# Performance work log

Hardware: AMD Instinct MI355X
Metric: run time of the kernel (lower is better)

## Reference

```python
import jax, jax.numpy as jnp
import numpy as np

K_SIZE = 5
EPS = 1e-6
EPS_L = 1e-3
EPS_W = 1e-3


def setup_inputs() -> dict:
    key = jax.random.key(0)
    k1, k2, k3 = jax.random.split(key, 3)
    B, H, W = 4, 512, 512
    return {
        "input": jax.random.normal(k1, (B, 1, H, W), jnp.float32),
        "L_params": jax.random.normal(k2, (B, H, W, 3), jnp.float32),
        "w": jax.random.normal(k3, (B, 2, H, W), jnp.float32),
    }


def _bilinear(img, py, px):
    # img: (B,H,W); py,px: (B,K,H,W) absolute sample coords. Zero outside bounds
    # (matches torchvision deform_conv2d zero-padded bilinear sampling).
    B, H, W = img.shape
    y0 = jnp.floor(py)
    x0 = jnp.floor(px)
    wy = py - y0  # fractional weights
    wx = px - x0
    bidx = jnp.arange(B)[:, None, None, None]

    def corner(yc, xc, wgt):
        valid = (yc >= 0) & (yc <= H - 1) & (xc >= 0) & (xc <= W - 1)
        yi = jnp.clip(yc, 0, H - 1).astype(jnp.int32)
        xi = jnp.clip(xc, 0, W - 1).astype(jnp.int32)
        return jnp.where(valid, img[bidx, yi, xi] * wgt, 0.0)

    return (corner(y0, x0, (1 - wy) * (1 - wx))
            + corner(y0, x0 + 1, (1 - wy) * wx)
            + corner(y0 + 1, x0, wy * (1 - wx))
            + corner(y0 + 1, x0 + 1, wy * wx))


def reference(input, L_params, w):
    B, C, H, W = input.shape
    n = K_SIZE  # n_theta = ceil(sqrt(k*k)) = k

    # --- per-pixel 2x2 metric M = L L^T, L = [[a,0],[b,c]] ---
    a = jnp.abs(L_params[..., 0]) + EPS_L
    b = L_params[..., 1]
    c = jnp.abs(L_params[..., 2]) + EPS_L
    M00 = a * a            # (B,H,W)
    M01 = a * b            # = M10
    M11 = b * b + c * c

    # --- inverse of (M + eps*I), closed-form 2x2 ---
    d00 = M00 + EPS
    d11 = M11 + EPS
    det = d00 * d11 - M01 * M01
    I00 = d11 / det
    I01 = -M01 / det
    I11 = d00 / det

    # --- w rescaled so its M^{-1}-norm is < 1 (Randers condition) ---
    wx_ = w[:, 0]
    wy_ = w[:, 1]
    q = I00 * wx_ * wx_ + 2 * I01 * wx_ * wy_ + I11 * wy_ * wy_
    norm = jnp.sqrt(q + EPS)                                  # (B,H,W)
    tuned = (jax.nn.sigmoid(norm) - 0.5) * 2.0 * (1.0 - EPS_W)
    wt = w * (tuned / (norm + EPS))[:, None]                  # (B,2,H,W)

    # --- Randers unit-ball tangent sampling pattern ---
    theta = jnp.arange(0.0, 2.0 * np.pi - EPS, 2.0 * np.pi / n)  # (n,)
    ct = jnp.cos(theta)[None, :, None, None]  # (1,n,1,1)
    st = jnp.sin(theta)[None, :, None, None]
    # F(u) = sqrt(u^T M u) + <w,u>
    quad = (M00[:, None] * ct * ct + 2.0 * M01[:, None] * ct * st
            + M11[:, None] * st * st)                         # (B,n,H,W)
    F = jnp.sqrt(quad) + wt[:, 0:1] * ct + wt[:, 1:2] * st    # (B,n,H,W)
    yx = ct / (F + EPS)  # boundary point of unit Randers ball, x comp
    yy = st / (F + EPS)  # y comp

    s_interp = (jnp.arange(n, dtype=jnp.float32) + 1.0) / n   # (n,)
    s5 = s_interp[None, :, None, None, None]
    dy = (s5 * yy[:, None]).reshape(B, n * n, H, W)           # (B,K,H,W)
    dx = (s5 * yx[:, None]).reshape(B, n * n, H, W)

    gy = jnp.arange(H, dtype=jnp.float32)[None, None, :, None] + dy
    gx = jnp.arange(W, dtype=jnp.float32)[None, None, None, :] + dx

    samp = _bilinear(input[:, 0], gy, gx)                     # (B,K,H,W)
    # uniform deform-conv kernel weight 1/n^2; sample_centre=False => no centre term
    out = samp.sum(axis=1)[:, None] / float(n * n)            # (B,1,H,W)
    return out
```

## Files before the change

### kernel.cpp

```cpp
#include <hip/hip_runtime.h>
#include <math.h>

#define K_SIZE 5
#define EPS    1e-6f
#define EPS_L  1e-3f
#define EPS_W  1e-3f

#define BATCH 4
#define HGT   512
#define WID   512
#define HW    (HGT * WID)

#define ENT        513
#define ROW_ENTRIES 520
#define ROW_BYTES  (ROW_ENTRIES * 8)
#define IMG_BYTES  (ENT * ROW_BYTES)
#define TBL_BYTES  ((size_t)BATCH * IMG_BYTES)

typedef int int32x4 __attribute__((ext_vector_type(4)));
typedef float floatx2 __attribute__((ext_vector_type(2)));
typedef _Float16 half4v __attribute__((ext_vector_type(4)));
typedef _Float16 half2v __attribute__((ext_vector_type(2)));

__device__ float llvm_amdgcn_raw_buffer_load_fp32(int32x4 srsrc, int voffset,
                                                  int soffset, int aux)
    __asm("llvm.amdgcn.raw.buffer.load.f32");
__device__ floatx2 llvm_amdgcn_raw_buffer_load_2fp32(int32x4 srsrc, int voffset,
                                                     int soffset, int aux)
    __asm("llvm.amdgcn.raw.buffer.load.v2f32");

__global__ __launch_bounds__(256) void pack_kernel(
    const float* __restrict__ input, char* __restrict__ tbl)
{
    const int t = blockIdx.x * blockDim.x + threadIdx.x;
    if (t >= BATCH * ENT * ENT) return;
    const int k  = t % ENT;
    const int ri = (t / ENT) % ENT;
    const int b  = t / (ENT * ENT);

    const float* __restrict__ img = input + (size_t)b * HW;

    const bool top = (ri >= 1), bot = (ri <= HGT - 1);
    const bool lef = (k  >= 1), rig = (k  <= WID - 1);
    const int yT = (ri - 1) << 9;
    const int yB = ri << 9;

    union { half4v h; floatx2 f; } cv;
    cv.h.x = (_Float16)((top && lef) ? img[yT + k - 1] : 0.0f);
    cv.h.y = (_Float16)((top && rig) ? img[yT + k]     : 0.0f);
    cv.h.z = (_Float16)((bot && lef) ? img[yB + k - 1] : 0.0f);
    cv.h.w = (_Float16)((bot && rig) ? img[yB + k]     : 0.0f);

    floatx2* dst = (floatx2*)(tbl + (size_t)b * IMG_BYTES + (size_t)ri * ROW_BYTES + ((size_t)k << 3));
    *dst = cv.f;
}

__global__ __launch_bounds__(256) void fused_sample_kernel_f16(
    const char* __restrict__ tbl,
    const float* __restrict__ Lp,
    const float* __restrict__ wbuf,
    float* __restrict__ out)
{
#pragma clang fp contract(off)
    const int idx = blockIdx.x * blockDim.x + threadIdx.x;

    const int b = blockIdx.x >> 10;
    const int p = idx & (HW - 1);
    const int y = p >> 9;
    const int x = p & (WID - 1);

    union {
        struct { const void* base; unsigned num; unsigned cfg; } s;
        int32x4 v;
    } desc;
    desc.s.base = (const void*)(tbl + (size_t)b * IMG_BYTES);
    desc.s.num  = (unsigned)IMG_BYTES;
    desc.s.cfg  = 0x00020000u;
    const int32x4 rsrc = desc.v;

    const size_t l_off = (size_t)idx * 3;
    const float L0 = Lp[l_off + 0];
    const float L1 = Lp[l_off + 1];
    const float L2 = Lp[l_off + 2];

    const float a  = fabsf(L0) + EPS_L;
    const float bb = L1;
    const float c  = fabsf(L2) + EPS_L;

    const float M00 = a * a;
    const float M01 = a * bb;
    const float M11 = (bb * bb) + (c * c);

    const float d00 = M00 + EPS;
    const float d11 = M11 + EPS;
    const float det = (d00 * d11) - (M01 * M01);
    const float I00 = d11 / det;
    const float I01 = (-M01) / det;
    const float I11 = d00 / det;

    const float wx = wbuf[(size_t)b * 2 * HW + p];
    const float wy = wbuf[(size_t)b * 2 * HW + HW + p];

    const float q    = (((I00 * wx) * wx) + (((2.0f * I01) * wx) * wy)) + ((I11 * wy) * wy);
    const float norm = sqrtf(q + EPS);

    const float e    = (float)exp((double)(-norm));
    const float sig  = 1.0f / (1.0f + e);
    const float tuned = ((sig - 0.5f) * 2.0f) * (1.0f - EPS_W);
    const float scale = tuned / (norm + EPS);
    const float wtx = wx * scale;
    const float wty = wy * scale;

    const float CT[K_SIZE] = { 1.0f,  0.30901696090f, -0.80901703575f, -0.80901693229f,  0.30901712828f };
    const float ST[K_SIZE] = { 0.0f,  0.95105652717f,  0.58778519534f, -0.58778533774f, -0.95105647279f };
    const float SV[K_SIZE] = { 0.2f, 0.4f, 0.6f, 0.8f, 1.0f };

    const float fy = (float)y;
    const float fx = (float)x;

    float acc0 = 0.0f;
    float acc1 = 0.0f;

    #pragma unroll
    for (int k = 0; k < K_SIZE; ++k) {
        const float ct = CT[k];
        const float st = ST[k];
        const float quad = (((M00 * ct) * ct) + (((2.0f * M01) * ct) * st)) + ((M11 * st) * st);
        const float F    = (sqrtf(quad) + (wtx * ct)) + (wty * st);
        const float Fe   = F + EPS;
        const float rFe  = __builtin_amdgcn_rcpf(Fe);
        const float yx   = ct * rFe;
        const float yy   = st * rFe;

        #pragma unroll
        for (int s = 0; s < K_SIZE; ++s) {
            const float sv = SV[s];
            const float gy = fmaf(sv, yy, fy);
            const float gx = fmaf(sv, yx, fx);

            const int   y0i = (int)floorf(gy);
            const int   x0i = (int)floorf(gx);
            const float wyf = __builtin_amdgcn_fractf(gy);
            const float wxf = __builtin_amdgcn_fractf(gx);

            const int ri = y0i + 1;
            const int ke = min(max(x0i + 1, 0), ENT - 1);
            const unsigned off = (unsigned)ri * (unsigned)ROW_BYTES + ((unsigned)ke << 3);

            const floatx2 pf = llvm_amdgcn_raw_buffer_load_2fp32(rsrc, (int)off, 0, 0);
            union { floatx2 f; half4v h; } cv;
            cv.f = pf;
            const float v00 = (float)cv.h.x;
            const float v01 = (float)cv.h.y;
            const float v10 = (float)cv.h.z;
            const float v11 = (float)cv.h.w;

            const bool vx0 = (unsigned)x0i < (unsigned)WID;
            const bool vx1 = (unsigned)(x0i + 1) < (unsigned)WID;
            const float zx0 = vx0 ? (1.0f - wxf) : 0.0f;
            const float zx1 = vx1 ? wxf : 0.0f;

            const float row0 = fmaf(v01, zx1, v00 * zx0);
            const float row1 = fmaf(v11, zx1, v10 * zx0);

            if (s & 1) {
                acc1 = fmaf(1.0f - wyf, row0, acc1);
                acc1 = fmaf(wyf,        row1, acc1);
            } else {
                acc0 = fmaf(1.0f - wyf, row0, acc0);
                acc0 = fmaf(wyf,        row1, acc0);
            }
        }
    }

    out[idx] = (acc0 + acc1) / (float)(K_SIZE * K_SIZE);
}

__global__ __launch_bounds__(256) void fused_sample_kernel_f32(
    const float* __restrict__ input,
    const float* __restrict__ Lp,
    const float* __restrict__ wbuf,
    float* __restrict__ out)
{
#pragma clang fp contract(off)
    const int idx = blockIdx.x * blockDim.x + threadIdx.x;
    const int b = blockIdx.x >> 10;
    const int p = idx & (HW - 1);
    const int y = p >> 9;
    const int x = p & (WID - 1);

    union {
        struct { const void* base; unsigned num; unsigned cfg; } s;
        int32x4 v;
    } desc;
    desc.s.base = (const void*)(input + (size_t)b * HW);
    desc.s.num  = HW * 4u;
    desc.s.cfg  = 0x00020000u;
    const int32x4 rsrc = desc.v;

    const size_t l_off = (size_t)idx * 3;
    const float L0 = Lp[l_off + 0];
    const float L1 = Lp[l_off + 1];
    const float L2 = Lp[l_off + 2];

    const float a  = fabsf(L0) + EPS_L;
    const float bb = L1;
    const float c  = fabsf(L2) + EPS_L;

    const float M00 = a * a;
    const float M01 = a * bb;
    const float M11 = (bb * bb) + (c * c);

    const float d00 = M00 + EPS;
    const float d11 = M11 + EPS;
    const float det = (d00 * d11) - (M01 * M01);
    const float I00 = d11 / det;
    const float I01 = (-M01) / det;
    const float I11 = d00 / det;

    const float wx = wbuf[(size_t)b * 2 * HW + p];
    const float wy = wbuf[(size_t)b * 2 * HW + HW + p];

    const float q    = (((I00 * wx) * wx) + (((2.0f * I01) * wx) * wy)) + ((I11 * wy) * wy);
    const float norm = sqrtf(q + EPS);
    const float e    = (float)exp((double)(-norm));
    const float sig  = 1.0f / (1.0f + e);
    const float tuned = ((sig - 0.5f) * 2.0f) * (1.0f - EPS_W);
    const float scale = tuned / (norm + EPS);
    const float wtx = wx * scale;
    const float wty = wy * scale;

    const float CT[K_SIZE] = { 1.0f,  0.30901696090f, -0.80901703575f, -0.80901693229f,  0.30901712828f };
    const float ST[K_SIZE] = { 0.0f,  0.95105652717f,  0.58778519534f, -0.58778533774f, -0.95105647279f };
    const float SV[K_SIZE] = { 0.2f, 0.4f, 0.6f, 0.8f, 1.0f };

    const float fy = (float)y;
    const float fx = (float)x;

    float acc0 = 0.0f;
    float acc1 = 0.0f;

    #pragma unroll
    for (int k = 0; k < K_SIZE; ++k) {
        const float ct = CT[k];
        const float st = ST[k];
        const float quad = (((M00 * ct) * ct) + (((2.0f * M01) * ct) * st)) + ((M11 * st) * st);
        const float F    = (sqrtf(quad) + (wtx * ct)) + (wty * st);
        const float Fe   = F + EPS;
        const float rFe  = __builtin_amdgcn_rcpf(Fe);
        const float yx   = ct * rFe;
        const float yy   = st * rFe;

        #pragma unroll
        for (int s = 0; s < K_SIZE; ++s) {
            const float sv = SV[s];
            const float gy = fmaf(sv, yy, fy);
            const float gx = fmaf(sv, yx, fx);

            const int   y0i = (int)floorf(gy);
            const int   x0i = (int)floorf(gx);
            const float wyf = __builtin_amdgcn_fractf(gy);
            const float wxf = __builtin_amdgcn_fractf(gx);

            const unsigned r0 = (unsigned)y0i << 11;
            const unsigned r1 = r0 + (WID * 4u);

            const int x1i = x0i + 1;
            const bool vx0 = (unsigned)x0i < (unsigned)WID;
            const bool vx1 = (unsigned)x1i < (unsigned)WID;
            const unsigned x0v = (unsigned)min(max(x0i, 0), WID - 1) << 2;
            const unsigned x1v = (unsigned)min(max(x1i, 0), WID - 1) << 2;

            const float v00 = llvm_amdgcn_raw_buffer_load_fp32(rsrc, (int)(r0 + x0v), 0, 0);
            const float v01 = llvm_amdgcn_raw_buffer_load_fp32(rsrc, (int)(r0 + x1v), 0, 0);
            const float v10 = llvm_amdgcn_raw_buffer_load_fp32(rsrc, (int)(r1 + x0v), 0, 0);
            const float v11 = llvm_amdgcn_raw_buffer_load_fp32(rsrc, (int)(r1 + x1v), 0, 0);

            const float zx0 = vx0 ? (1.0f - wxf) : 0.0f;
            const float zx1 = vx1 ? wxf : 0.0f;

            const float row0 = fmaf(v01, zx1, v00 * zx0);
            const float row1 = fmaf(v11, zx1, v10 * zx0);

            if (s & 1) {
                acc1 = fmaf(1.0f - wyf, row0, acc1);
                acc1 = fmaf(wyf,        row1, acc1);
            } else {
                acc0 = fmaf(1.0f - wyf, row0, acc0);
                acc0 = fmaf(wyf,        row1, acc0);
            }
        }
    }

    out[idx] = (acc0 + acc1) / (float)(K_SIZE * K_SIZE);
}

extern "C" void kernel_launch(void* const* d_in, const int* in_sizes, int n_in,
                              void* d_out, int out_size, void* d_ws, size_t ws_size,
                              hipStream_t stream) {
    const float* input = (const float*)d_in[0];
    const float* Lp    = (const float*)d_in[1];
    const float* wbuf  = (const float*)d_in[2];
    float* out = (float*)d_out;

    if (ws_size >= TBL_BYTES) {
        char* tbl = (char*)d_ws;
        const int pack_total = BATCH * ENT * ENT;
        pack_kernel<<<(pack_total + 255) / 256, 256, 0, stream>>>(input, tbl);
        fused_sample_kernel_f16<<<BATCH * HW / 256, 256, 0, stream>>>(tbl, Lp, wbuf, out);
    } else {
        fused_sample_kernel_f32<<<BATCH * HW / 256, 256, 0, stream>>>(input, Lp, wbuf, out);
    }
}
```

Before: 39.86 us.

## Stage per-block window of packed bilinear table into shared memory

Each 256-thread block, which covers half an image row, cooperatively loads a 12x268 window of the packed fp16 corner table into LDS and then serves the 25 bilinear gathers per pixel from LDS. A global buffer load is kept as a fallback for samples that fall outside the window. The aim is to replace scattered global/L2 gathers with LDS reads. In exchange it adds about 25 KB of LDS per block, which may limit occupancy, plus a barrier, window bounds checks and possibly divergent fallback loads.

```diff
diff --git a/kernel.cpp b/kernel.cpp
--- a/kernel.cpp
+++ b/kernel.cpp
@@ -17,10 +17,14 @@
 #define IMG_BYTES  (ENT * ROW_BYTES)
 #define TBL_BYTES  ((size_t)BATCH * IMG_BYTES)
 
+#define WROWS 12
+#define WCOLS 268
+#define WR_OFF 5
+#define WC_OFF 5
+
 typedef int int32x4 __attribute__((ext_vector_type(4)));
 typedef float floatx2 __attribute__((ext_vector_type(2)));
 typedef _Float16 half4v __attribute__((ext_vector_type(4)));
-typedef _Float16 half2v __attribute__((ext_vector_type(2)));
 
 __device__ float llvm_amdgcn_raw_buffer_load_fp32(int32x4 srsrc, int voffset,
                                                   int soffset, int aux)
@@ -62,12 +66,18 @@
     float* __restrict__ out)
 {
 #pragma clang fp contract(off)
+    __shared__ floatx2 tile[WROWS * WCOLS];
+
     const int idx = blockIdx.x * blockDim.x + threadIdx.x;
 
     const int b = blockIdx.x >> 10;
     const int p = idx & (HW - 1);
     const int y = p >> 9;
     const int x = p & (WID - 1);
+
+    const int xs    = (blockIdx.x & 1) << 8;
+    const int rbase = y - WR_OFF;
+    const int kbase = xs - WC_OFF;
 
     union {
         struct { const void* base; unsigned num; unsigned cfg; } s;
@@ -78,6 +88,15 @@
     desc.s.cfg  = 0x00020000u;
     const int32x4 rsrc = desc.v;
 
+    for (int i = threadIdx.x; i < WROWS * WCOLS; i += 256) {
+        const int rr = i / WCOLS;
+        const int kk = i - rr * WCOLS;
+        const int ri = rbase + rr;
+        const int k  = kbase + kk;
+        const unsigned off = (unsigned)(ri * ROW_BYTES + (k << 3));
+        tile[i] = llvm_amdgcn_raw_buffer_load_2fp32(rsrc, (int)off, 0, 0);
+    }
+
     const size_t l_off = (size_t)idx * 3;
     const float L0 = Lp[l_off + 0];
     const float L1 = Lp[l_off + 1];
@@ -120,6 +139,8 @@
 
     float acc0 = 0.0f;
     float acc1 = 0.0f;
+
+    __syncthreads();
 
     #pragma unroll
     for (int k = 0; k < K_SIZE; ++k) {
@@ -145,11 +166,23 @@
 
             const int ri = y0i + 1;
             const int ke = min(max(x0i + 1, 0), ENT - 1);
-            const unsigned off = (unsigned)ri * (unsigned)ROW_BYTES + ((unsigned)ke << 3);
-
-            const floatx2 pf = llvm_amdgcn_raw_buffer_load_2fp32(rsrc, (int)off, 0, 0);
+
+            const int iri = ri - rbase;
+            const int ike = ke - kbase;
+            const bool inWin = ((unsigned)iri < (unsigned)WROWS) &
+                               ((unsigned)ike < (unsigned)WCOLS);
+            const int lidx = min(max(iri, 0), WROWS - 1) * WCOLS
+                           + min(max(ike, 0), WCOLS - 1);
+
+            floatx2 qv = tile[lidx];
+            if (!inWin) {
+                const unsigned off = (unsigned)ri * (unsigned)ROW_BYTES
+                                   + ((unsigned)ke << 3);
+                qv = llvm_amdgcn_raw_buffer_load_2fp32(rsrc, (int)off, 0, 0);
+            }
+
             union { floatx2 f; half4v h; } cv;
-            cv.f = pf;
+            cv.f = qv;
             const float v00 = (float)cv.h.x;
             const float v01 = (float)cv.h.y;
             const float v10 = (float)cv.h.z;
```

After: 64.39 us. 61.6% more time.
